# Optimization experiments

Hardware: AMD Instinct MI355X
Metric: run time of the kernel (lower is better)

The kernel has to match this reference:

```python
import jax, jax.numpy as jnp
import numpy as np

N = 150000      # nodes per branch
E = 2400000     # edges per branch (avg degree 16)
G = 128         # graphs in batch
F_IN, H, EMB = 3, 128, 512
BN_EPS = 1e-5


def setup_inputs() -> dict:
    key = jax.random.key(0)
    ks = jax.random.split(key, 24)
    inp = {
        "x1": jax.random.normal(ks[0], (N, F_IN), jnp.float32),
        "edge_index1": jax.random.randint(ks[1], (2, E), 0, N, jnp.int32),
        "batch1": jnp.sort(jax.random.randint(ks[2], (N,), 0, G, jnp.int32)),
        "x2": jax.random.normal(ks[3], (N, F_IN), jnp.float32),
        "edge_index2": jax.random.randint(ks[4], (2, E), 0, N, jnp.int32),
        "batch2": jnp.sort(jax.random.randint(ks[5], (N,), 0, G, jnp.int32)),
        # GCNConv weights (PyG: out = norm-agg(x @ W) + b), shared (siamese)
        "W1": jax.random.normal(ks[6], (F_IN, H), jnp.float32) / np.sqrt(F_IN),
        "b1": jnp.zeros((H,), jnp.float32),
        "W2": jax.random.normal(ks[7], (H, H), jnp.float32) / np.sqrt(H),
        "b2": jnp.zeros((H,), jnp.float32),
        "W3": jax.random.normal(ks[8], (H, H), jnp.float32) / np.sqrt(H),
        "b3": jnp.zeros((H,), jnp.float32),
        # BatchNorm affine params
        "g1": jnp.ones((H,), jnp.float32), "be1": jnp.zeros((H,), jnp.float32),
        "g2": jnp.ones((H,), jnp.float32), "be2": jnp.zeros((H,), jnp.float32),
        # projection MLP
        "Wp1": jax.random.normal(ks[9], (H, H), jnp.float32) / np.sqrt(H),
        "bp1": jnp.zeros((H,), jnp.float32),
        "Wp2": jax.random.normal(ks[10], (H, EMB), jnp.float32) / np.sqrt(H),
        "bp2": jnp.zeros((EMB,), jnp.float32),
    }
    return inp


def gcn_conv(x, edge_index, W, b):
    """PyG GCNConv: add self-loops, symmetric D^-1/2 (A+I) D^-1/2 normalization."""
    n = x.shape[0]
    loop = jnp.arange(n, dtype=edge_index.dtype)
    src = jnp.concatenate([edge_index[0], loop])
    dst = jnp.concatenate([edge_index[1], loop])
    deg = jax.ops.segment_sum(jnp.ones_like(dst, jnp.float32), dst, num_segments=n)
    dinv = jnp.where(deg > 0, jax.lax.rsqrt(deg), 0.0)
    norm = dinv[src] * dinv[dst]                      # [E+N]
    h = x @ W                                         # [N,H] dense transform first
    msg = h[src] * norm[:, None]                      # gather + scale
    out = jax.ops.segment_sum(msg, dst, num_segments=n)  # scatter-add
    return out + b


def batch_norm(x, gamma, beta):
    mu = jnp.mean(x, axis=0)
    var = jnp.mean(jnp.square(x - mu), axis=0)  # biased, training-mode stats
    return (x - mu) * jax.lax.rsqrt(var + BN_EPS) * gamma + beta


def global_mean_pool(x, batch, num_graphs):
    sums = jax.ops.segment_sum(x, batch, num_segments=num_graphs)
    cnt = jax.ops.segment_sum(jnp.ones((x.shape[0],), x.dtype), batch, num_segments=num_graphs)
    return sums / jnp.maximum(cnt, 1.0)[:, None]


def forward_once(x, edge_index, batch, W1, b1, W2, b2, W3, b3, g1, be1, g2, be2, Wp1, bp1, Wp2, bp2):
    x = jax.nn.relu(batch_norm(gcn_conv(x, edge_index, W1, b1), g1, be1))
    x = jax.nn.relu(batch_norm(gcn_conv(x, edge_index, W2, b2), g2, be2))
    x = gcn_conv(x, edge_index, W3, b3)
    x = global_mean_pool(x, batch, G)                 # [G,H]
    x = jax.nn.relu(x @ Wp1 + bp1) @ Wp2 + bp2        # [G,EMB]
    nrm = jnp.linalg.norm(x, axis=1, keepdims=True)
    return x / jnp.maximum(nrm, 1e-12)                # F.normalize(p=2, dim=1)


def reference(x1, edge_index1, batch1, x2, edge_index2, batch2,
              W1, b1, W2, b2, W3, b3, g1, be1, g2, be2, Wp1, bp1, Wp2, bp2):
    params = (W1, b1, W2, b2, W3, b3, g1, be1, g2, be2, Wp1, bp1, Wp2, bp2)
    out1 = forward_once(x1, edge_index1, batch1, *params)
    out2 = forward_once(x2, edge_index2, batch2, *params)
    return (out1, out2)
```

## Files before the change

### kernel.cpp

```cpp
#include <hip/hip_runtime.h>
#include <math.h>

#define BUCKET_SHIFT 8
#define BUCKET_MASK 255
#define MAXBUCK 640
#define TILE 8192

typedef __attribute__((ext_vector_type(8))) short bf16x8;
typedef __attribute__((ext_vector_type(4))) float f32x4;

__device__ inline float bf_lo(unsigned u) { return __uint_as_float(u << 16); }
__device__ inline float bf_hi(unsigned u) { return __uint_as_float(u & 0xffff0000u); }
__device__ inline float bf2f(unsigned short s) { return __uint_as_float((unsigned)s << 16); }
__device__ inline unsigned short f2bf(float f) {
  unsigned u = __float_as_uint(f);
  return (unsigned short)((u + 0x7fffu + ((u >> 16) & 1u)) >> 16);
}
__device__ inline void acc8(float* a, uint4 v) {
  a[0] += bf_lo(v.x); a[1] += bf_hi(v.x);
  a[2] += bf_lo(v.y); a[3] += bf_hi(v.y);
  a[4] += bf_lo(v.z); a[5] += bf_hi(v.z);
  a[6] += bf_lo(v.w); a[7] += bf_hi(v.w);
}
__device__ inline unsigned pack2(float a, float b) {
  return (unsigned)f2bf(a) | ((unsigned)f2bf(b) << 16);
}

__global__ void zero_u32(unsigned int* __restrict__ p, int n) {
  int i = blockIdx.x * blockDim.x + threadIdx.x;
  if (i < n) p[i] = 0u;
}

__global__ __launch_bounds__(256) void bucket_count(const int* __restrict__ dst0,
                                                    const int* __restrict__ dst1,
                                                    int* __restrict__ bcnt, int e, int nbuck) {
  int br = blockIdx.y;
  const int* dst = br ? dst1 : dst0;
  bcnt += (size_t)br * nbuck;
  __shared__ int lc[MAXBUCK];
  for (int i = threadIdx.x; i < nbuck; i += 256) lc[i] = 0;
  __syncthreads();
  for (int i = blockIdx.x * blockDim.x + threadIdx.x; i < e; i += gridDim.x * blockDim.x)
    atomicAdd(&lc[dst[i] >> BUCKET_SHIFT], 1);
  __syncthreads();
  for (int i = threadIdx.x; i < nbuck; i += 256)
    if (lc[i]) atomicAdd(&bcnt[i], lc[i]);
}

__global__ __launch_bounds__(1024) void bucket_scan(const int* __restrict__ bcnt,
                                                    int* __restrict__ bbase,
                                                    int* __restrict__ bcur, int nbuck) {
  int br = blockIdx.y;
  bcnt += (size_t)br * nbuck;
  bbase += (size_t)br * (nbuck + 1);
  bcur += (size_t)br * nbuck;
  __shared__ int s[1024];
  int t = threadIdx.x;
  int v = (t < nbuck) ? bcnt[t] : 0;
  s[t] = v;
  __syncthreads();
  for (int off = 1; off < 1024; off <<= 1) {
    int u = (t >= off) ? s[t - off] : 0;
    __syncthreads();
    s[t] += u;
    __syncthreads();
  }
  int excl = s[t] - v;
  if (t < nbuck) {
    bbase[t] = excl;
    bcur[t] = excl;
  } else if (t == nbuck) {
    bbase[t] = excl;
  }
}

__global__ __launch_bounds__(256) void bucket_scatter(const int* __restrict__ src0,
                                                      const int* __restrict__ dst0,
                                                      const int* __restrict__ src1,
                                                      const int* __restrict__ dst1,
                                                      int* __restrict__ bcur,
                                                      int* __restrict__ bucketed,
                                                      int e, int nbuck) {
  int br = blockIdx.y;
  const int* src = br ? src1 : src0;
  const int* dst = br ? dst1 : dst0;
  bcur += (size_t)br * nbuck;
  bucketed += (size_t)br * e;
  __shared__ int lcnt[MAXBUCK], gb[MAXBUCK];
  int t = threadIdx.x;
  int tile0 = blockIdx.x * TILE;
  int tn = min(TILE, e - tile0);
  for (int i = t; i < nbuck; i += 256) lcnt[i] = 0;
  __syncthreads();
  for (int i = t; i < tn; i += 256)
    atomicAdd(&lcnt[dst[tile0 + i] >> BUCKET_SHIFT], 1);
  __syncthreads();
  for (int i = t; i < nbuck; i += 256) {
    int c = lcnt[i];
    gb[i] = c ? atomicAdd(&bcur[i], c) : 0;
  }
  __syncthreads();
  for (int i = t; i < nbuck; i += 256) lcnt[i] = 0;
  __syncthreads();
  for (int i = t; i < tn; i += 256) {
    int d = dst[tile0 + i];
    int s = src[tile0 + i];
    int b = d >> BUCKET_SHIFT;
    int r = atomicAdd(&lcnt[b], 1);
    bucketed[gb[b] + r] = (s << 8) | (d & BUCKET_MASK);
  }
}

__global__ __launch_bounds__(256) void bucket_to_csr(const int* __restrict__ bucketed,
                                                     const int* __restrict__ bbase,
                                                     int* __restrict__ rp,
                                                     float* __restrict__ dinv,
                                                     int* __restrict__ csr,
                                                     int n, int e, int nbuck) {
  int br = blockIdx.y;
  bucketed += (size_t)br * e;
  bbase += (size_t)br * (nbuck + 1);
  rp += (size_t)br * (n + 1);
  dinv += (size_t)br * n;
  csr += (size_t)br * e;
  __shared__ int lcnt[256], lrp[256];
  int b = blockIdx.x, t = threadIdx.x;
  int n0 = b << BUCKET_SHIFT;
  int base = bbase[b];
  int cnt_e = bbase[b + 1] - base;
  lcnt[t] = 0;
  __syncthreads();
  for (int i = t; i < cnt_e; i += 256)
    atomicAdd(&lcnt[bucketed[base + i] & BUCKET_MASK], 1);
  __syncthreads();
  int v = lcnt[t];
  lrp[t] = v;
  __syncthreads();
  for (int off = 1; off < 256; off <<= 1) {
    int u = (t >= off) ? lrp[t - off] : 0;
    __syncthreads();
    lrp[t] += u;
    __syncthreads();
  }
  int excl = lrp[t] - v;
  int node = n0 + t;
  if (node < n) {
    rp[node] = base + excl;
    dinv[node] = rsqrtf((float)v + 1.0f);
  }
  if (b == nbuck - 1 && t == 0) rp[n] = e;
  lrp[t] = excl;
  lcnt[t] = 0;
  __syncthreads();
  for (int i = t; i < cnt_e; i += 256) {
    int ed = bucketed[base + i];
    int li = ed & BUCKET_MASK;
    int pos = atomicAdd(&lcnt[li], 1);
    csr[base + lrp[li] + pos] = (int)(((unsigned)ed) >> 8);
  }
}

__global__ void graph_bounds(const int* __restrict__ batch0, const int* __restrict__ batch1,
                             int* __restrict__ gstart, int n, int g) {
  int br = blockIdx.y;
  const int* batch = br ? batch1 : batch0;
  gstart += (size_t)br * (g + 1);
  int i = blockIdx.x * blockDim.x + threadIdx.x;
  if (i >= n) return;
  int b = batch[i];
  int bp = (i == 0) ? -1 : batch[i - 1];
  for (int k = bp + 1; k <= b; ++k) gstart[k] = i;
  if (i == n - 1)
    for (int k = b + 1; k <= g; ++k) gstart[k] = n;
}

__global__ void xs_scale(const float* __restrict__ x0, const float* __restrict__ x1,
                         const float* __restrict__ dinv, float4* __restrict__ xs, int n) {
  int br = blockIdx.y;
  const float* x = br ? x1 : x0;
  dinv += (size_t)br * n;
  xs += (size_t)br * n;
  int i = blockIdx.x * blockDim.x + threadIdx.x;
  if (i >= n) return;
  float d = dinv[i];
  xs[i] = make_float4(x[3 * (size_t)i] * d, x[3 * (size_t)i + 1] * d,
                      x[3 * (size_t)i + 2] * d, d);
}

__global__ __launch_bounds__(256) void agg_f3(const float4* __restrict__ xs,
                                              const int* __restrict__ rp,
                                              const int* __restrict__ csr,
                                              const float* __restrict__ dinv,
                                              float4* __restrict__ out,
                                              float* __restrict__ mpart, int n, int e, int nb3) {
  int br = blockIdx.y;
  xs += (size_t)br * n;
  rp += (size_t)br * (n + 1);
  csr += (size_t)br * e;
  dinv += (size_t)br * n;
  out += (size_t)br * n;
  mpart += (size_t)br * nb3 * 9;
  int i = blockIdx.x * blockDim.x + threadIdx.x;
  int t = threadIdx.x;
  float a0 = 0.f, a1 = 0.f, a2 = 0.f;
  if (i < n) {
    float4 self = xs[i];
    a0 = self.x; a1 = self.y; a2 = self.z;
    int e0 = rp[i], e1 = rp[i + 1];
    int ee = e0;
    for (; ee + 4 <= e1; ee += 4) {
      int s0 = csr[ee], s1 = csr[ee + 1], s2 = csr[ee + 2], s3 = csr[ee + 3];
      float4 v0 = xs[s0], v1 = xs[s1], v2 = xs[s2], v3 = xs[s3];
      a0 += (v0.x + v1.x) + (v2.x + v3.x);
      a1 += (v0.y + v1.y) + (v2.y + v3.y);
      a2 += (v0.z + v1.z) + (v2.z + v3.z);
    }
    for (; ee < e1; ++ee) {
      float4 v = xs[csr[ee]];
      a0 += v.x; a1 += v.y; a2 += v.z;
    }
    float d = dinv[i];
    a0 *= d; a1 *= d; a2 *= d;
    out[i] = make_float4(a0, a1, a2, 0.f);
  }
  float loc[9] = {a0, a1, a2, a0 * a0, a0 * a1, a0 * a2, a1 * a1, a1 * a2, a2 * a2};
  __shared__ float red[256];
  for (int q = 0; q < 9; ++q) {
    red[t] = loc[q];
    __syncthreads();
    for (int s = 128; s > 0; s >>= 1) {
      if (t < s) red[t] += red[t + s];
      __syncthreads();
    }
    if (t == 0) mpart[blockIdx.x * 9 + q] = red[0];
    __syncthreads();
  }
}

__global__ void bnprep1(const float* __restrict__ mpart, int nblk,
                        const float* __restrict__ W1, const float* __restrict__ b1,
                        const float* __restrict__ g1, const float* __restrict__ be1,
                        float invn, float4* __restrict__ W1r, float2* __restrict__ prm) {
  int br = blockIdx.y;
  mpart += (size_t)br * nblk * 9;
  W1r += (size_t)br * 128;
  prm += (size_t)br * 128;
  __shared__ float red[256];
  __shared__ float sm[9];
  int t = threadIdx.x;
  float loc[9] = {0.f, 0.f, 0.f, 0.f, 0.f, 0.f, 0.f, 0.f, 0.f};
  for (int i = t; i < nblk; i += 256)
#pragma unroll
    for (int q = 0; q < 9; ++q) loc[q] += mpart[i * 9 + q];
  for (int q = 0; q < 9; ++q) {
    red[t] = loc[q];
    __syncthreads();
    for (int s = 128; s > 0; s >>= 1) {
      if (t < s) red[t] += red[t + s];
      __syncthreads();
    }
    if (t == 0) sm[q] = red[0] * invn;
    __syncthreads();
  }
  if (t < 128) {
    float w0 = W1[t], w1 = W1[128 + t], w2 = W1[256 + t], b = b1[t];
    float mu0 = sm[0] * w0 + sm[1] * w1 + sm[2] * w2;
    float q2 = w0 * w0 * sm[3] + w1 * w1 * sm[6] + w2 * w2 * sm[8]
             + 2.f * (w0 * w1 * sm[4] + w0 * w2 * sm[5] + w1 * w2 * sm[7]);
    float var = q2 - mu0 * mu0;
    float sc = rsqrtf(fmaxf(var, 0.f) + 1e-5f) * g1[t];
    float mu = mu0 + b;
    W1r[t] = make_float4(w0, w1, w2, b);
    prm[t] = make_float2(sc, be1[t] - mu * sc);
  }
}

__global__ void wsplit2(const float* __restrict__ W2, const float* __restrict__ W3,
                        unsigned short* __restrict__ Wf2, unsigned short* __restrict__ Wf3) {
  const float* W = blockIdx.y ? W3 : W2;
  unsigned short* Wf = blockIdx.y ? Wf3 : Wf2;
  int i = blockIdx.x * 256 + threadIdx.x;
  if (i >= 128 * 128) return;
  int k = i >> 7, f = i & 127;
  float w = W[i];
  unsigned short hi = f2bf(w);
  float hif = __uint_as_float((unsigned)hi << 16);
  unsigned short lo = f2bf(w - hif);
  int NT = f >> 4, l15 = f & 15, ks = k >> 5, lg = (k >> 3) & 3, j = k & 7;
  int lane = lg * 16 + l15;
  size_t base = ((size_t)(NT * 4 + ks) * 64 + lane) * 8 + j;
  Wf[base] = hi;
  Wf[16384 + base] = lo;
}

template <int MODE>
__global__ __launch_bounds__(256) void gemm_mfma_t(const unsigned short* __restrict__ Abf,
                                                   const float4* __restrict__ ag0,
                                                   const float4* __restrict__ W1r,
                                                   const unsigned short* __restrict__ Wf,
                                                   const float* __restrict__ dinv,
                                                   const float2* __restrict__ prm,
                                                   unsigned short* __restrict__ C, int n) {
  int br = blockIdx.y;
  if (MODE == 1) Abf += (size_t)br * n * 128;
  if (MODE == 2) { ag0 += (size_t)br * n; W1r += (size_t)br * 128; }
  dinv += (size_t)br * n;
  C += (size_t)br * n * 128;
  prm += (size_t)br * 128;
  const int t = threadIdx.x;
  const int wave = t >> 6, lane = t & 63;
  const int l15 = lane & 15, lg = lane >> 4;
  const int row0 = blockIdx.x * 128 + wave * 32;
  const int n0 = row0 + l15, n1 = row0 + 16 + l15;
  const bf16x8* wfr = (const bf16x8*)Wf;
  float4 a0v = make_float4(0.f, 0.f, 0.f, 0.f), a1v = a0v;
  if (MODE == 2) {
    if (n0 < n) a0v = ag0[n0];
    if (n1 < n) a1v = ag0[n1];
  }
  f32x4 acc[8][2] = {};
#pragma unroll
  for (int ks = 0; ks < 4; ++ks) {
    int k0 = ks * 32 + lg * 8;
    bf16x8 nf0 = {}, nf1 = {};
    if (MODE == 1) {
      if (n0 < n) nf0 = *(const bf16x8*)&Abf[(size_t)n0 * 128 + k0];
      if (n1 < n) nf1 = *(const bf16x8*)&Abf[(size_t)n1 * 128 + k0];
      float4 pa = *(const float4*)&prm[k0];
      float4 pb = *(const float4*)&prm[k0 + 2];
      float4 pc = *(const float4*)&prm[k0 + 4];
      float4 pd = *(const float4*)&prm[k0 + 6];
      float scv[8] = {pa.x, pa.z, pb.x, pb.z, pc.x, pc.z, pd.x, pd.z};
      float ofv[8] = {pa.y, pa.w, pb.y, pb.w, pc.y, pc.w, pd.y, pd.w};
#pragma unroll
      for (int j = 0; j < 8; ++j) {
        float x0 = fmaxf(bf2f((unsigned short)nf0[j]) * scv[j] + ofv[j], 0.f);
        float x1 = fmaxf(bf2f((unsigned short)nf1[j]) * scv[j] + ofv[j], 0.f);
        nf0[j] = (short)f2bf(x0);
        nf1[j] = (short)f2bf(x1);
      }
    } else {
#pragma unroll
      for (int j = 0; j < 8; ++j) {
        int f = k0 + j;
        float4 wv = W1r[f];
        float2 p = prm[f];
        float x0 = (a0v.x * wv.x + a0v.y * wv.y + a0v.z * wv.z + wv.w) * p.x + p.y;
        float x1 = (a1v.x * wv.x + a1v.y * wv.y + a1v.z * wv.z + wv.w) * p.x + p.y;
        nf0[j] = (short)f2bf(fmaxf(x0, 0.f));
        nf1[j] = (short)f2bf(fmaxf(x1, 0.f));
      }
    }
#pragma unroll
    for (int NT = 0; NT < 8; ++NT) {
      bf16x8 wh = wfr[(NT * 4 + ks) * 64 + lane];
      bf16x8 wl = wfr[2048 + (NT * 4 + ks) * 64 + lane];
      acc[NT][0] = __builtin_amdgcn_mfma_f32_16x16x32_bf16(wh, nf0, acc[NT][0], 0, 0, 0);
      acc[NT][0] = __builtin_amdgcn_mfma_f32_16x16x32_bf16(wl, nf0, acc[NT][0], 0, 0, 0);
      acc[NT][1] = __builtin_amdgcn_mfma_f32_16x16x32_bf16(wh, nf1, acc[NT][1], 0, 0, 0);
      acc[NT][1] = __builtin_amdgcn_mfma_f32_16x16x32_bf16(wl, nf1, acc[NT][1], 0, 0, 0);
    }
  }
  float sc0 = (n0 < n) ? dinv[n0] : 0.f;
  float sc1 = (n1 < n) ? dinv[n1] : 0.f;
#pragma unroll
  for (int ng = 0; ng < 2; ++ng) {
    int node = (ng == 0) ? n0 : n1;
    float sc = (ng == 0) ? sc0 : sc1;
    if (node < n) {
#pragma unroll
      for (int NT = 0; NT < 8; ++NT) {
        ushort4 o;
        o.x = f2bf(acc[NT][ng][0] * sc);
        o.y = f2bf(acc[NT][ng][1] * sc);
        o.z = f2bf(acc[NT][ng][2] * sc);
        o.w = f2bf(acc[NT][ng][3] * sc);
        *(ushort4*)&C[(size_t)node * 128 + NT * 16 + lg * 4] = o;
      }
    }
  }
}

__global__ __launch_bounds__(256) void agg128_l2(const unsigned short* __restrict__ h,
                                                 const int* __restrict__ rp,
                                                 const int* __restrict__ csr,
                                                 const float* __restrict__ dinv,
                                                 const float* __restrict__ bias,
                                                 unsigned short* __restrict__ outb,
                                                 float* __restrict__ mpart, int n, int e,
                                                 int nagg) {
  int br = blockIdx.y;
  h += (size_t)br * n * 128;
  rp += (size_t)br * (n + 1);
  csr += (size_t)br * e;
  dinv += (size_t)br * n;
  outb += (size_t)br * n * 128;
  mpart += (size_t)br * nagg * 256;
  int t = threadIdx.x;
  int node = blockIdx.x * 16 + (t >> 4);
  int lane = t & 15;
  bool valid = node < n;
  const uint4* hp = (const uint4*)h;
  float acc[8] = {0.f};
  if (valid) {
    acc8(acc, hp[(size_t)node * 16 + lane]);
    int e0 = rp[node], e1 = rp[node + 1];
    int ee = e0;
    for (; ee + 8 <= e1; ee += 8) {
      int s0 = csr[ee],     s1 = csr[ee + 1], s2 = csr[ee + 2], s3 = csr[ee + 3];
      int s4 = csr[ee + 4], s5 = csr[ee + 5], s6 = csr[ee + 6], s7 = csr[ee + 7];
      uint4 v0 = hp[(size_t)s0 * 16 + lane];
      uint4 v1 = hp[(size_t)s1 * 16 + lane];
      uint4 v2 = hp[(size_t)s2 * 16 + lane];
      uint4 v3 = hp[(size_t)s3 * 16 + lane];
      uint4 v4 = hp[(size_t)s4 * 16 + lane];
      uint4 v5 = hp[(size_t)s5 * 16 + lane];
      uint4 v6 = hp[(size_t)s6 * 16 + lane];
      uint4 v7 = hp[(size_t)s7 * 16 + lane];
      acc8(acc, v0); acc8(acc, v1); acc8(acc, v2); acc8(acc, v3);
      acc8(acc, v4); acc8(acc, v5); acc8(acc, v6); acc8(acc, v7);
    }
    for (; ee + 4 <= e1; ee += 4) {
      int s0 = csr[ee], s1 = csr[ee + 1], s2 = csr[ee + 2], s3 = csr[ee + 3];
      uint4 v0 = hp[(size_t)s0 * 16 + lane];
      uint4 v1 = hp[(size_t)s1 * 16 + lane];
      uint4 v2 = hp[(size_t)s2 * 16 + lane];
      uint4 v3 = hp[(size_t)s3 * 16 + lane];
      acc8(acc, v0); acc8(acc, v1); acc8(acc, v2); acc8(acc, v3);
    }
    for (; ee < e1; ++ee) acc8(acc, hp[(size_t)csr[ee] * 16 + lane]);
  }
  float v[8], sq[8];
  if (valid) {
    float dd = dinv[node];
    float4 bb0 = *(const float4*)&bias[lane * 8];
    float4 bb1 = *(const float4*)&bias[lane * 8 + 4];
    v[0] = acc[0] * dd + bb0.x; v[1] = acc[1] * dd + bb0.y;
    v[2] = acc[2] * dd + bb0.z; v[3] = acc[3] * dd + bb0.w;
    v[4] = acc[4] * dd + bb1.x; v[5] = acc[5] * dd + bb1.y;
    v[6] = acc[6] * dd + bb1.z; v[7] = acc[7] * dd + bb1.w;
    uint4 o;
    o.x = pack2(v[0], v[1]); o.y = pack2(v[2], v[3]);
    o.z = pack2(v[4], v[5]); o.w = pack2(v[6], v[7]);
    *(uint4*)&outb[(size_t)node * 128 + lane * 8] = o;
  } else {
#pragma unroll
    for (int j = 0; j < 8; ++j) v[j] = 0.f;
  }
#pragma unroll
  for (int j = 0; j < 8; ++j) sq[j] = v[j] * v[j];
#pragma unroll
  for (int j = 0; j < 8; ++j) {
    v[j] += __shfl_xor(v[j], 16);  v[j] += __shfl_xor(v[j], 32);
    sq[j] += __shfl_xor(sq[j], 16); sq[j] += __shfl_xor(sq[j], 32);
  }
  __shared__ float sred[4][16][16];
  int wave = t >> 6, wl = t & 63;
  if (wl < 16) {
#pragma unroll
    for (int j = 0; j < 8; ++j) {
      sred[wave][wl][j] = v[j];
      sred[wave][wl][8 + j] = sq[j];
    }
  }
  __syncthreads();
  {
    int f = t & 127;
    int j = (f & 7) + ((t >> 7) << 3);
    float s = sred[0][f >> 3][j] + sred[1][f >> 3][j]
            + sred[2][f >> 3][j] + sred[3][f >> 3][j];
    mpart[(size_t)blockIdx.x * 256 + t] = s;
  }
}

__global__ __launch_bounds__(256) void bnred1(const float* __restrict__ mpart, int nblk,
                                              float* __restrict__ spart) {
  int br = blockIdx.y;
  mpart += (size_t)br * nblk * 256;
  spart += (size_t)br * 128 * 256;
  int t = threadIdx.x, b = blockIdx.x;
  float loc = 0.f;
  for (int i = b; i < nblk; i += 128) loc += mpart[(size_t)i * 256 + t];
  spart[b * 256 + t] = loc;
}

__global__ void bnprep2(const float* __restrict__ spart,
                        const float* __restrict__ gam, const float* __restrict__ bet,
                        float invn, float2* __restrict__ prm) {
  int br = blockIdx.y;
  spart += (size_t)br * 128 * 256;
  prm += (size_t)br * 128;
  int t = threadIdx.x;
  float loc = 0.f;
  for (int i = 0; i < 128; ++i) loc += spart[i * 256 + t];
  __shared__ float sm[256];
  sm[t] = loc;
  __syncthreads();
  if (t < 128) {
    float mu = sm[t] * invn;
    float var = sm[128 + t] * invn - mu * mu;
    float sc = rsqrtf(fmaxf(var, 0.f) + 1e-5f) * gam[t];
    prm[t] = make_float2(sc, bet[t] - mu * sc);
  }
}

__global__ __launch_bounds__(256) void agg128_l3_pool(const unsigned short* __restrict__ h,
                                                      const int* __restrict__ rp,
                                                      const int* __restrict__ csr,
                                                      const float* __restrict__ dinv,
                                                      const float* __restrict__ bias,
                                                      const int* __restrict__ batch0,
                                                      const int* __restrict__ batch1,
                                                      float* __restrict__ pooled,
                                                      int n, int e, int g) {
  int br = blockIdx.y;
  h += (size_t)br * n * 128;
  rp += (size_t)br * (n + 1);
  csr += (size_t)br * e;
  dinv += (size_t)br * n;
  const int* batch = br ? batch1 : batch0;
  pooled += (size_t)br * g * 128;
  int t = threadIdx.x;
  int node = blockIdx.x * 16 + (t >> 4);
  int lane = t & 15;
  bool valid = node < n;
  const uint4* hp = (const uint4*)h;
  float acc[8] = {0.f};
  if (valid) {
    acc8(acc, hp[(size_t)node * 16 + lane]);
    int e0 = rp[node], e1 = rp[node + 1];
    int ee = e0;
    for (; ee + 8 <= e1; ee += 8) {
      int s0 = csr[ee],     s1 = csr[ee + 1], s2 = csr[ee + 2], s3 = csr[ee + 3];
      int s4 = csr[ee + 4], s5 = csr[ee + 5], s6 = csr[ee + 6], s7 = csr[ee + 7];
      uint4 v0 = hp[(size_t)s0 * 16 + lane];
      uint4 v1 = hp[(size_t)s1 * 16 + lane];
      uint4 v2 = hp[(size_t)s2 * 16 + lane];
      uint4 v3 = hp[(size_t)s3 * 16 + lane];
      uint4 v4 = hp[(size_t)s4 * 16 + lane];
      uint4 v5 = hp[(size_t)s5 * 16 + lane];
      uint4 v6 = hp[(size_t)s6 * 16 + lane];
      uint4 v7 = hp[(size_t)s7 * 16 + lane];
      acc8(acc, v0); acc8(acc, v1); acc8(acc, v2); acc8(acc, v3);
      acc8(acc, v4); acc8(acc, v5); acc8(acc, v6); acc8(acc, v7);
    }
    for (; ee + 4 <= e1; ee += 4) {
      int s0 = csr[ee], s1 = csr[ee + 1], s2 = csr[ee + 2], s3 = csr[ee + 3];
      uint4 v0 = hp[(size_t)s0 * 16 + lane];
      uint4 v1 = hp[(size_t)s1 * 16 + lane];
      uint4 v2 = hp[(size_t)s2 * 16 + lane];
      uint4 v3 = hp[(size_t)s3 * 16 + lane];
      acc8(acc, v0); acc8(acc, v1); acc8(acc, v2); acc8(acc, v3);
    }
    for (; ee < e1; ++ee) acc8(acc, hp[(size_t)csr[ee] * 16 + lane]);
  }
  __shared__ float lds[16][128];
  __shared__ int lgid[16];
  int ng = t >> 4;
  if (valid) {
    float dd = dinv[node];
    float4 bb0 = *(const float4*)&bias[lane * 8];
    float4 bb1 = *(const float4*)&bias[lane * 8 + 4];
    float w0 = bf2f(f2bf(acc[0] * dd + bb0.x));
    float w1 = bf2f(f2bf(acc[1] * dd + bb0.y));
    float w2 = bf2f(f2bf(acc[2] * dd + bb0.z));
    float w3 = bf2f(f2bf(acc[3] * dd + bb0.w));
    float w4 = bf2f(f2bf(acc[4] * dd + bb1.x));
    float w5 = bf2f(f2bf(acc[5] * dd + bb1.y));
    float w6 = bf2f(f2bf(acc[6] * dd + bb1.z));
    float w7 = bf2f(f2bf(acc[7] * dd + bb1.w));
    lds[ng][lane * 8 + 0] = w0; lds[ng][lane * 8 + 1] = w1;
    lds[ng][lane * 8 + 2] = w2; lds[ng][lane * 8 + 3] = w3;
    lds[ng][lane * 8 + 4] = w4; lds[ng][lane * 8 + 5] = w5;
    lds[ng][lane * 8 + 6] = w6; lds[ng][lane * 8 + 7] = w7;
    if (lane == 0) lgid[ng] = batch[node];
  } else {
#pragma unroll
    for (int j = 0; j < 8; ++j) lds[ng][lane * 8 + j] = 0.f;
    if (lane == 0) lgid[ng] = -1;
  }
  __syncthreads();
  {
    int f = t & 127, half = t >> 7;
    int lo = half * 8, hi = lo + 8;
    float run = 0.f;
    int cur = lgid[lo];
    for (int k = lo; k < hi; ++k) {
      int gg = lgid[k];
      if (gg != cur) {
        if (cur >= 0 && run != 0.f) atomicAdd(&pooled[cur * 128 + f], run);
        run = 0.f;
        cur = gg;
      }
      run += lds[k][f];
    }
    if (cur >= 0 && run != 0.f) atomicAdd(&pooled[cur * 128 + f], run);
  }
}

__global__ void mlp_kernel(const float* __restrict__ pooled, const int* __restrict__ gstart,
                           const float* __restrict__ Wp1, const float* __restrict__ bp1,
                           const float* __restrict__ Wp2, const float* __restrict__ bp2,
                           float* __restrict__ out, int g) {
  int br = blockIdx.y;
  pooled += (size_t)br * g * 128;
  gstart += (size_t)br * (g + 1);
  out += (size_t)br * g * 512;
  int gg = blockIdx.x, t = threadIdx.x;
  __shared__ float pv[128], hid[128], ov[512], red[256];
  if (t < 128) {
    float cntf = (float)(gstart[gg + 1] - gstart[gg]);
    pv[t] = pooled[gg * 128 + t] / fmaxf(cntf, 1.0f);
  }
  __syncthreads();
  if (t < 128) {
    float a = bp1[t];
    for (int k = 0; k < 128; ++k) a += pv[k] * Wp1[k * 128 + t];
    hid[t] = fmaxf(a, 0.0f);
  }
  __syncthreads();
  for (int o = t; o < 512; o += 256) {
    float a = bp2[o];
    for (int k = 0; k < 128; ++k) a += hid[k] * Wp2[k * 512 + o];
    ov[o] = a;
  }
  __syncthreads();
  red[t] = ov[t] * ov[t] + ov[t + 256] * ov[t + 256];
  __syncthreads();
  for (int sdt = 128; sdt > 0; sdt >>= 1) {
    if (t < sdt) red[t] += red[t + sdt];
    __syncthreads();
  }
  float inv = 1.0f / fmaxf(sqrtf(red[0]), 1e-12f);
  for (int o = t; o < 512; o += 256) out[(size_t)gg * 512 + o] = ov[o] * inv;
}

extern "C" void kernel_launch(void* const* d_in, const int* in_sizes, int n_in,
                              void* d_out, int out_size, void* d_ws, size_t ws_size,
                              hipStream_t stream) {
  const int N = in_sizes[0] / 3;
  const int E = in_sizes[1] / 2;
  const int G = out_size / (2 * 512);
  const int NBUCK = (N + BUCKET_MASK) >> BUCKET_SHIFT;
  const int NB3 = (N + 255) / 256;
  const int NAGG = (N + 15) / 16;

  char* w = (char*)d_ws;
  auto alloc = [&](size_t bytes) -> void* {
    void* p = (void*)w;
    w += (bytes + 255) & ~(size_t)255;
    return p;
  };
  unsigned short* Abf      = (unsigned short*)alloc(2 * (size_t)N * 128 * 2);
  unsigned short* Bh       = (unsigned short*)alloc(2 * (size_t)N * 128 * 2);
  float*          dinv     = (float*)alloc(2 * (size_t)N * 4);
  float4*         xs       = (float4*)alloc(2 * (size_t)N * 16);
  float4*         ag0      = (float4*)alloc(2 * (size_t)N * 16);
  int*            rp       = (int*)alloc(2 * (size_t)(N + 1) * 4);
  int*            csr      = (int*)alloc(2 * (size_t)E * 4);
  int*            bucketed = (int*)alloc(2 * (size_t)E * 4);
  int*            bcnt     = (int*)alloc(2 * (size_t)NBUCK * 4);
  int*            bbase    = (int*)alloc(2 * (size_t)(NBUCK + 1) * 4);
  int*            bcur     = (int*)alloc(2 * (size_t)NBUCK * 4);
  int*            gstart   = (int*)alloc(2 * (size_t)(G + 1) * 4);
  float*          pooled   = (float*)alloc(2 * (size_t)G * 128 * 4);
  unsigned short* Wf2      = (unsigned short*)alloc(2 * 128 * 128 * 2);
  unsigned short* Wf3      = (unsigned short*)alloc(2 * 128 * 128 * 2);
  float*          mpart    = (float*)alloc(2 * (size_t)NB3 * 9 * 4);
  float*          mpart2   = (float*)alloc(2 * (size_t)NAGG * 256 * 4);
  float*          spart    = (float*)alloc(2 * (size_t)128 * 256 * 4);
  float4*         W1r      = (float4*)alloc(2 * 128 * 16);
  float2*         prm1     = (float2*)alloc(2 * 128 * 8);
  float2*         prm2     = (float2*)alloc(2 * 128 * 8);

  const float* x0    = (const float*)d_in[0];
  const int*   ei0   = (const int*)d_in[1];
  const int*   bat0  = (const int*)d_in[2];
  const float* x1    = (const float*)d_in[3];
  const int*   ei1   = (const int*)d_in[4];
  const int*   bat1  = (const int*)d_in[5];
  const float* W1  = (const float*)d_in[6];
  const float* b1  = (const float*)d_in[7];
  const float* W2  = (const float*)d_in[8];
  const float* b2  = (const float*)d_in[9];
  const float* W3  = (const float*)d_in[10];
  const float* b3  = (const float*)d_in[11];
  const float* g1  = (const float*)d_in[12];
  const float* be1 = (const float*)d_in[13];
  const float* g2  = (const float*)d_in[14];
  const float* be2 = (const float*)d_in[15];
  const float* Wp1 = (const float*)d_in[16];
  const float* bp1 = (const float*)d_in[17];
  const float* Wp2 = (const float*)d_in[18];
  const float* bp2 = (const float*)d_in[19];

  const int* src0 = ei0;
  const int* dst0 = ei0 + E;
  const int* src1 = ei1;
  const int* dst1 = ei1 + E;
  float* outp = (float*)d_out;

  const int TB = 256;
  const int NTILE = (E + TILE - 1) / TILE;
  const float invn = 1.0f / (float)N;

  wsplit2<<<dim3(64, 2), TB, 0, stream>>>(W2, W3, Wf2, Wf3);

  zero_u32<<<(2 * NBUCK + TB - 1) / TB, TB, 0, stream>>>((unsigned*)bcnt, 2 * NBUCK);
  bucket_count<<<dim3(256, 2), TB, 0, stream>>>(dst0, dst1, bcnt, E, NBUCK);
  bucket_scan<<<dim3(1, 2), 1024, 0, stream>>>(bcnt, bbase, bcur, NBUCK);
  bucket_scatter<<<dim3(NTILE, 2), TB, 0, stream>>>(src0, dst0, src1, dst1, bcur, bucketed, E, NBUCK);
  bucket_to_csr<<<dim3(NBUCK, 2), TB, 0, stream>>>(bucketed, bbase, rp, dinv, csr, N, E, NBUCK);

  graph_bounds<<<dim3((N + TB - 1) / TB, 2), TB, 0, stream>>>(bat0, bat1, gstart, N, G);

  xs_scale<<<dim3((N + TB - 1) / TB, 2), TB, 0, stream>>>(x0, x1, dinv, xs, N);
  agg_f3<<<dim3(NB3, 2), TB, 0, stream>>>(xs, rp, csr, dinv, ag0, mpart, N, E, NB3);
  bnprep1<<<dim3(1, 2), TB, 0, stream>>>(mpart, NB3, W1, b1, g1, be1, invn, W1r, prm1);

  gemm_mfma_t<2><<<dim3((N + 127) / 128, 2), TB, 0, stream>>>(nullptr, ag0, W1r, Wf2, dinv, prm1, Bh, N);
  agg128_l2<<<dim3(NAGG, 2), TB, 0, stream>>>(Bh, rp, csr, dinv, b2, Abf, mpart2, N, E, NAGG);
  bnred1<<<dim3(128, 2), TB, 0, stream>>>(mpart2, NAGG, spart);
  bnprep2<<<dim3(1, 2), TB, 0, stream>>>(spart, g2, be2, invn, prm2);

  gemm_mfma_t<1><<<dim3((N + 127) / 128, 2), TB, 0, stream>>>(Abf, nullptr, nullptr, Wf3, dinv, prm2, Bh, N);
  zero_u32<<<(2 * G * 128 + TB - 1) / TB, TB, 0, stream>>>((unsigned*)pooled, 2 * G * 128);
  agg128_l3_pool<<<dim3(NAGG, 2), TB, 0, stream>>>(Bh, rp, csr, dinv, b3, bat0, bat1, pooled, N, E, G);

  mlp_kernel<<<dim3(G, 2), TB, 0, stream>>>(pooled, gstart, Wp1, bp1, Wp2, bp2, outp, G);
}
```

Measured before the change: 727.2 us.

## Cut kernel launches: fold scans into consumers, merge prep kernels, single zero pass

```diff
diff --git a/kernel.cpp b/kernel.cpp
--- a/kernel.cpp
+++ b/kernel.cpp
@@ -47,57 +47,52 @@
     if (lc[i]) atomicAdd(&bcnt[i], lc[i]);
 }
 
-__global__ __launch_bounds__(1024) void bucket_scan(const int* __restrict__ bcnt,
-                                                    int* __restrict__ bbase,
-                                                    int* __restrict__ bcur, int nbuck) {
-  int br = blockIdx.y;
-  bcnt += (size_t)br * nbuck;
-  bbase += (size_t)br * (nbuck + 1);
-  bcur += (size_t)br * nbuck;
-  __shared__ int s[1024];
-  int t = threadIdx.x;
-  int v = (t < nbuck) ? bcnt[t] : 0;
-  s[t] = v;
-  __syncthreads();
-  for (int off = 1; off < 1024; off <<= 1) {
-    int u = (t >= off) ? s[t - off] : 0;
-    __syncthreads();
-    s[t] += u;
-    __syncthreads();
-  }
-  int excl = s[t] - v;
-  if (t < nbuck) {
-    bbase[t] = excl;
-    bcur[t] = excl;
-  } else if (t == nbuck) {
-    bbase[t] = excl;
-  }
-}
-
 __global__ __launch_bounds__(256) void bucket_scatter(const int* __restrict__ src0,
                                                       const int* __restrict__ dst0,
                                                       const int* __restrict__ src1,
                                                       const int* __restrict__ dst1,
+                                                      const int* __restrict__ bcnt,
                                                       int* __restrict__ bcur,
                                                       int* __restrict__ bucketed,
                                                       int e, int nbuck) {
   int br = blockIdx.y;
   const int* src = br ? src1 : src0;
   const int* dst = br ? dst1 : dst0;
+  bcnt += (size_t)br * nbuck;
   bcur += (size_t)br * nbuck;
   bucketed += (size_t)br * e;
-  __shared__ int lcnt[MAXBUCK], gb[MAXBUCK];
+  __shared__ int sbase[MAXBUCK], lcnt[MAXBUCK], gb[MAXBUCK];
+  __shared__ int stmp[256];
+  __shared__ int scarry;
   int t = threadIdx.x;
   int tile0 = blockIdx.x * TILE;
   int tn = min(TILE, e - tile0);
+  if (t == 0) scarry = 0;
   for (int i = t; i < nbuck; i += 256) lcnt[i] = 0;
   __syncthreads();
+  for (int c0 = 0; c0 < nbuck; c0 += 256) {
+    int idx = c0 + t;
+    int v = (idx < nbuck) ? bcnt[idx] : 0;
+    stmp[t] = v;
+    __syncthreads();
+    for (int off = 1; off < 256; off <<= 1) {
+      int u = (t >= off) ? stmp[t - off] : 0;
+      __syncthreads();
+      stmp[t] += u;
+      __syncthreads();
+    }
+    int excl = stmp[t] - v + scarry;
+    if (idx < nbuck) sbase[idx] = excl;
+    __syncthreads();
+    if (t == 255) scarry += stmp[255];
+    __syncthreads();
+  }
   for (int i = t; i < tn; i += 256)
     atomicAdd(&lcnt[dst[tile0 + i] >> BUCKET_SHIFT], 1);
   __syncthreads();
   for (int i = t; i < nbuck; i += 256) {
     int c = lcnt[i];
-    gb[i] = c ? atomicAdd(&bcur[i], c) : 0;
+    gb[i] = c ? sbase[i] + atomicAdd(&bcur[i], c) : 0;
   }
   __syncthreads();
   for (int i = t; i < nbuck; i += 256) lcnt[i] = 0;
@@ -112,22 +107,35 @@
 }
 
 __global__ __launch_bounds__(256) void bucket_to_csr(const int* __restrict__ bucketed,
-                                                     const int* __restrict__ bbase,
+                                                     const int* __restrict__ bcnt,
                                                      int* __restrict__ rp,
                                                      float* __restrict__ dinv,
                                                      int* __restrict__ csr,
                                                      int n, int e, int nbuck) {
   int br = blockIdx.y;
   bucketed += (size_t)br * e;
-  bbase += (size_t)br * (nbuck + 1);
+  bcnt += (size_t)br * nbuck;
   rp += (size_t)br * (n + 1);
   dinv += (size_t)br * n;
   csr += (size_t)br * e;
   __shared__ int lcnt[256], lrp[256];
+  __shared__ int sbb;
   int b = blockIdx.x, t = threadIdx.x;
   int n0 = b << BUCKET_SHIFT;
-  int base = bbase[b];
-  int cnt_e = bbase[b + 1] - base;
+  {
+    int part = 0;
+    for (int i = t; i < b; i += 256) part += bcnt[i];
+    lrp[t] = part;
+    __syncthreads();
+    for (int s = 128; s > 0; s >>= 1) {
+      if (t < s) lrp[t] += lrp[t + s];
+      __syncthreads();
+    }
+    if (t == 0) sbb = lrp[0];
+    __syncthreads();
+  }
+  int base = sbb;
+  int cnt_e = bcnt[b];
   lcnt[t] = 0;
   __syncthreads();
   for (int i = t; i < cnt_e; i += 256)
@@ -160,31 +168,26 @@
   }
 }
 
-__global__ void graph_bounds(const int* __restrict__ batch0, const int* __restrict__ batch1,
-                             int* __restrict__ gstart, int n, int g) {
-  int br = blockIdx.y;
+__global__ void prep(const float* __restrict__ x0, const float* __restrict__ x1,
+                     const int* __restrict__ batch0, const int* __restrict__ batch1,
+                     const float* __restrict__ dinv, float4* __restrict__ xs,
+                     int* __restrict__ gstart, int n, int g) {
+  int br = blockIdx.y;
+  const float* x = br ? x1 : x0;
   const int* batch = br ? batch1 : batch0;
+  dinv += (size_t)br * n;
+  xs += (size_t)br * n;
   gstart += (size_t)br * (g + 1);
   int i = blockIdx.x * blockDim.x + threadIdx.x;
   if (i >= n) return;
+  float d = dinv[i];
+  xs[i] = make_float4(x[3 * (size_t)i] * d, x[3 * (size_t)i + 1] * d,
+                      x[3 * (size_t)i + 2] * d, d);
   int b = batch[i];
   int bp = (i == 0) ? -1 : batch[i - 1];
   for (int k = bp + 1; k <= b; ++k) gstart[k] = i;
   if (i == n - 1)
     for (int k = b + 1; k <= g; ++k) gstart[k] = n;
-}
-
-__global__ void xs_scale(const float* __restrict__ x0, const float* __restrict__ x1,
-                         const float* __restrict__ dinv, float4* __restrict__ xs, int n) {
-  int br = blockIdx.y;
-  const float* x = br ? x1 : x0;
-  dinv += (size_t)br * n;
-  xs += (size_t)br * n;
-  int i = blockIdx.x * blockDim.x + threadIdx.x;
-  if (i >= n) return;
-  float d = dinv[i];
-  xs[i] = make_float4(x[3 * (size_t)i] * d, x[3 * (size_t)i + 1] * d,
-                      x[3 * (size_t)i + 2] * d, d);
 }
 
 __global__ __launch_bounds__(256) void agg_f3(const float4* __restrict__ xs,
@@ -208,6 +211,15 @@
     a0 = self.x; a1 = self.y; a2 = self.z;
     int e0 = rp[i], e1 = rp[i + 1];
     int ee = e0;
+    for (; ee + 8 <= e1; ee += 8) {
+      int s0 = csr[ee],     s1 = csr[ee + 1], s2 = csr[ee + 2], s3 = csr[ee + 3];
+      int s4 = csr[ee + 4], s5 = csr[ee + 5], s6 = csr[ee + 6], s7 = csr[ee + 7];
+      float4 v0 = xs[s0], v1 = xs[s1], v2 = xs[s2], v3 = xs[s3];
+      float4 v4 = xs[s4], v5 = xs[s5], v6 = xs[s6], v7 = xs[s7];
+      a0 += ((v0.x + v1.x) + (v2.x + v3.x)) + ((v4.x + v5.x) + (v6.x + v7.x));
+      a1 += ((v0.y + v1.y) + (v2.y + v3.y)) + ((v4.y + v5.y) + (v6.y + v7.y));
+      a2 += ((v0.z + v1.z) + (v2.z + v3.z)) + ((v4.z + v5.z) + (v6.z + v7.z));
+    }
     for (; ee + 4 <= e1; ee += 4) {
       int s0 = csr[ee], s1 = csr[ee + 1], s2 = csr[ee + 2], s3 = csr[ee + 3];
       float4 v0 = xs[s0], v1 = xs[s1], v2 = xs[s2], v3 = xs[s3];
@@ -240,11 +252,10 @@
 __global__ void bnprep1(const float* __restrict__ mpart, int nblk,
                         const float* __restrict__ W1, const float* __restrict__ b1,
                         const float* __restrict__ g1, const float* __restrict__ be1,
-                        float invn, float4* __restrict__ W1r, float2* __restrict__ prm) {
+                        float invn, float4* __restrict__ W1s) {
   int br = blockIdx.y;
   mpart += (size_t)br * nblk * 9;
-  W1r += (size_t)br * 128;
-  prm += (size_t)br * 128;
+  W1s += (size_t)br * 128;
   __shared__ float red[256];
   __shared__ float sm[9];
   int t = threadIdx.x;
@@ -263,15 +274,13 @@
     __syncthreads();
   }
   if (t < 128) {
-    float w0 = W1[t], w1 = W1[128 + t], w2 = W1[256 + t], b = b1[t];
+    float w0 = W1[t], w1 = W1[128 + t], w2 = W1[256 + t];
     float mu0 = sm[0] * w0 + sm[1] * w1 + sm[2] * w2;
     float q2 = w0 * w0 * sm[3] + w1 * w1 * sm[6] + w2 * w2 * sm[8]
              + 2.f * (w0 * w1 * sm[4] + w0 * w2 * sm[5] + w1 * w2 * sm[7]);
     float var = q2 - mu0 * mu0;
     float sc = rsqrtf(fmaxf(var, 0.f) + 1e-5f) * g1[t];
-    float mu = mu0 + b;
-    W1r[t] = make_float4(w0, w1, w2, b);
-    prm[t] = make_float2(sc, be1[t] - mu * sc);
+    W1s[t] = make_float4(w0 * sc, w1 * sc, w2 * sc, be1[t] - mu0 * sc);
   }
 }
 
@@ -296,17 +305,16 @@
 template <int MODE>
 __global__ __launch_bounds__(256) void gemm_mfma_t(const unsigned short* __restrict__ Abf,
                                                    const float4* __restrict__ ag0,
-                                                   const float4* __restrict__ W1r,
+                                                   const float4* __restrict__ W1s,
                                                    const unsigned short* __restrict__ Wf,
                                                    const float* __restrict__ dinv,
                                                    const float2* __restrict__ prm,
                                                    unsigned short* __restrict__ C, int n) {
   int br = blockIdx.y;
-  if (MODE == 1) Abf += (size_t)br * n * 128;
-  if (MODE == 2) { ag0 += (size_t)br * n; W1r += (size_t)br * 128; }
+  if (MODE == 1) { Abf += (size_t)br * n * 128; prm += (size_t)br * 128; }
+  if (MODE == 2) { ag0 += (size_t)br * n; W1s += (size_t)br * 128; }
   dinv += (size_t)br * n;
   C += (size_t)br * n * 128;
-  prm += (size_t)br * 128;
   const int t = threadIdx.x;
   const int wave = t >> 6, lane = t & 63;
   const int l15 = lane & 15, lg = lane >> 4;
@@ -343,10 +351,9 @@
 #pragma unroll
       for (int j = 0; j < 8; ++j) {
         int f = k0 + j;
-        float4 wv = W1r[f];
-        float2 p = prm[f];
-        float x0 = (a0v.x * wv.x + a0v.y * wv.y + a0v.z * wv.z + wv.w) * p.x + p.y;
-        float x1 = (a1v.x * wv.x + a1v.y * wv.y + a1v.z * wv.z + wv.w) * p.x + p.y;
+        float4 wv = W1s[f];
+        float x0 = a0v.x * wv.x + a0v.y * wv.y + a0v.z * wv.z + wv.w;
+        float x1 = a1v.x * wv.x + a1v.y * wv.y + a1v.z * wv.z + wv.w;
         nf0[j] = (short)f2bf(fmaxf(x0, 0.f));
         nf1[j] = (short)f2bf(fmaxf(x1, 0.f));
       }
@@ -477,10 +484,10 @@
                                               float* __restrict__ spart) {
   int br = blockIdx.y;
   mpart += (size_t)br * nblk * 256;
-  spart += (size_t)br * 128 * 256;
+  spart += (size_t)br * 32 * 256;
   int t = threadIdx.x, b = blockIdx.x;
   float loc = 0.f;
-  for (int i = b; i < nblk; i += 128) loc += mpart[(size_t)i * 256 + t];
+  for (int i = b; i < nblk; i += 32) loc += mpart[(size_t)i * 256 + t];
   spart[b * 256 + t] = loc;
 }
 
@@ -488,11 +495,11 @@
                         const float* __restrict__ gam, const float* __restrict__ bet,
                         float invn, float2* __restrict__ prm) {
   int br = blockIdx.y;
-  spart += (size_t)br * 128 * 256;
+  spart += (size_t)br * 32 * 256;
   prm += (size_t)br * 128;
   int t = threadIdx.x;
   float loc = 0.f;
-  for (int i = 0; i < 128; ++i) loc += spart[i * 256 + t];
+  for (int i = 0; i < 32; ++i) loc += spart[i * 256 + t];
   __shared__ float sm[256];
   sm[t] = loc;
   __syncthreads();
@@ -651,6 +658,10 @@
     w += (bytes + 255) & ~(size_t)255;
     return p;
   };
+  int*            bcnt     = (int*)alloc(2 * (size_t)NBUCK * 4);
+  int*            bcur     = (int*)alloc(2 * (size_t)NBUCK * 4);
+  float*          pooled   = (float*)alloc(2 * (size_t)G * 128 * 4);
+  char*           zend     = w;
   unsigned short* Abf      = (unsigned short*)alloc(2 * (size_t)N * 128 * 2);
   unsigned short* Bh       = (unsigned short*)alloc(2 * (size_t)N * 128 * 2);
   float*          dinv     = (float*)alloc(2 * (size_t)N * 4);
@@ -659,18 +670,13 @@
   int*            rp       = (int*)alloc(2 * (size_t)(N + 1) * 4);
   int*            csr      = (int*)alloc(2 * (size_t)E * 4);
   int*            bucketed = (int*)alloc(2 * (size_t)E * 4);
-  int*            bcnt     = (int*)alloc(2 * (size_t)NBUCK * 4);
-  int*            bbase    = (int*)alloc(2 * (size_t)(NBUCK + 1) * 4);
-  int*            bcur     = (int*)alloc(2 * (size_t)NBUCK * 4);
   int*            gstart   = (int*)alloc(2 * (size_t)(G + 1) * 4);
-  float*          pooled   = (float*)alloc(2 * (size_t)G * 128 * 4);
   unsigned short* Wf2      = (unsigned short*)alloc(2 * 128 * 128 * 2);
   unsigned short* Wf3      = (unsigned short*)alloc(2 * 128 * 128 * 2);
   float*          mpart    = (float*)alloc(2 * (size_t)NB3 * 9 * 4);
   float*          mpart2   = (float*)alloc(2 * (size_t)NAGG * 256 * 4);
-  float*          spart    = (float*)alloc(2 * (size_t)128 * 256 * 4);
-  float4*         W1r      = (float4*)alloc(2 * 128 * 16);
-  float2*         prm1     = (float2*)alloc(2 * 128 * 8);
+  float*          spart    = (float*)alloc(2 * (size_t)32 * 256 * 4);
+  float4*         W1s      = (float4*)alloc(2 * 128 * 16);
   float2*         prm2     = (float2*)alloc(2 * 128 * 8);
 
   const float* x0    = (const float*)d_in[0];
@@ -703,29 +709,31 @@
   const int TB = 256;
   const int NTILE = (E + TILE - 1) / TILE;
   const float invn = 1.0f / (float)N;
-
+  const int zcnt = (int)((zend - (char*)bcnt) / 4);
+
+  zero_u32<<<(zcnt + TB - 1) / TB, TB, 0, stream>>>((unsigned*)bcnt, zcnt);
   wsplit2<<<dim3(64, 2), TB, 0, stream>>>(W2, W3, Wf2, Wf3);
 
-  zero_u32<<<(2 * NBUCK + TB - 1) / TB, TB, 0, stream>>>((unsigned*)bcnt, 2 * NBUCK);
   bucket_count<<<dim3(256, 2), TB, 0, stream>>>(dst0, dst1, bcnt, E, NBUCK);
-  bucket_scan<<<dim3(1, 2), 1024, 0, stream>>>(bcnt, bbase, bcur, NBUCK);
-  bucket_scatter<<<dim3(NTILE, 2), TB, 0, stream>>>(src0, dst0, src1, dst1, bcur, bucketed, E, NBUCK);
-  bucket_to_csr<<<dim3(NBUCK, 2), TB, 0, stream>>>(bucketed, bbase, rp, dinv, csr, N, E, NBUCK);
-
-  graph_bounds<<<dim3((N + TB - 1) / TB, 2), TB, 0, stream>>>(bat0, bat1, gstart, N, G);
-
-  xs_scale<<<dim3((N + TB - 1) / TB, 2), TB, 0, stream>>>(x0, x1, dinv, xs, N);
+  bucket_scatter<<<dim3(NTILE, 2), TB, 0, stream>>>(src0, dst0, src1, dst1, bcnt, bcur,
+                                                    bucketed, E, NBUCK);
+  bucket_to_csr<<<dim3(NBUCK, 2), TB, 0, stream>>>(bucketed, bcnt, rp, dinv, csr, N, E, NBUCK);
+
+  prep<<<dim3((N + TB - 1) / TB, 2), TB, 0, stream>>>(x0, x1, bat0, bat1, dinv, xs, gstart, N, G);
+
   agg_f3<<<dim3(NB3, 2), TB, 0, stream>>>(xs, rp, csr, dinv, ag0, mpart, N, E, NB3);
-  bnprep1<<<dim3(1, 2), TB, 0, stream>>>(mpart, NB3, W1, b1, g1, be1, invn, W1r, prm1);
-
-  gemm_mfma_t<2><<<dim3((N + 127) / 128, 2), TB, 0, stream>>>(nullptr, ag0, W1r, Wf2, dinv, prm1, Bh, N);
+  bnprep1<<<dim3(1, 2), TB, 0, stream>>>(mpart, NB3, W1, b1, g1, be1, invn, W1s);
+
+  gemm_mfma_t<2><<<dim3((N + 127) / 128, 2), TB, 0, stream>>>(nullptr, ag0, W1s, Wf2, dinv,
+                                                              nullptr, Bh, N);
   agg128_l2<<<dim3(NAGG, 2), TB, 0, stream>>>(Bh, rp, csr, dinv, b2, Abf, mpart2, N, E, NAGG);
-  bnred1<<<dim3(128, 2), TB, 0, stream>>>(mpart2, NAGG, spart);
+  bnred1<<<dim3(32, 2), TB, 0, stream>>>(mpart2, NAGG, spart);
   bnprep2<<<dim3(1, 2), TB, 0, stream>>>(spart, g2, be2, invn, prm2);
 
-  gemm_mfma_t<1><<<dim3((N + 127) / 128, 2), TB, 0, stream>>>(Abf, nullptr, nullptr, Wf3, dinv, prm2, Bh, N);
-  zero_u32<<<(2 * G * 128 + TB - 1) / TB, TB, 0, stream>>>((unsigned*)pooled, 2 * G * 128);
-  agg128_l3_pool<<<dim3(NAGG, 2), TB, 0, stream>>>(Bh, rp, csr, dinv, b3, bat0, bat1, pooled, N, E, G);
+  gemm_mfma_t<1><<<dim3((N + 127) / 128, 2), TB, 0, stream>>>(Abf, nullptr, nullptr, Wf3, dinv,
+                                                              prm2, Bh, N);
+  agg128_l3_pool<<<dim3(NAGG, 2), TB, 0, stream>>>(Bh, rp, csr, dinv, b3, bat0, bat1, pooled,
+                                                   N, E, G);
 
   mlp_kernel<<<dim3(G, 2), TB, 0, stream>>>(pooled, gstart, Wp1, bp1, Wp2, bp2, outp, G);
 }
```

Result: slower. 772.8 us (+6.3%).
